# Performance work log

Measured on AMD Instinct MI355X. Metric: run time of the kernel, lower is better.

The kernel has to match this reference:

```python
import jax, jax.numpy as jnp
import numpy as np

IOU_TR = 0.3
SCORE_TR = 0.1
EPS = 1e-9
N_DET = 4096
N_CLASSES = 20


def setup_inputs() -> dict:
    key = jax.random.key(0)
    k1, k2, k3, k4 = jax.random.split(key, 4)
    scores = jax.random.uniform(k1, (N_DET,), dtype=jnp.float32)
    classes = jax.random.randint(k2, (N_DET,), 0, N_CLASSES).astype(jnp.float32)
    centers = jax.random.uniform(k3, (N_DET, 3), dtype=jnp.float32) * 64.0
    dims = jax.random.uniform(k4, (N_DET, 3), dtype=jnp.float32) * 8.0 + 1.0
    results = jnp.concatenate([scores[:, None], classes[:, None], centers, dims], axis=1)
    return {"results": results}


def _pairwise_iou3d(boxes):
    # boxes: [N, 6] = (cx, cy, cz, w, h, d) center format
    c = boxes[:, :3]
    d = boxes[:, 3:]
    lo = c - d * 0.5  # [N,3]
    hi = c + d * 0.5
    inter_lo = jnp.maximum(lo[:, None, :], lo[None, :, :])  # [N,N,3]
    inter_hi = jnp.minimum(hi[:, None, :], hi[None, :, :])
    inter = jnp.prod(jnp.clip(inter_hi - inter_lo, 0.0, None), axis=-1)  # [N,N]
    vol = jnp.prod(d, axis=-1)  # [N]
    union = vol[:, None] + vol[None, :] - inter
    return inter / (union + EPS)


def reference(results):
    # results: [N, 8] = (score, class, cx, cy, cz, w, h, d)
    N = results.shape[0]
    order = jnp.argsort(-results[:, 0])  # sort by score descending
    r = results[order]
    valid = r[:, 0] >= SCORE_TR  # score threshold filter
    iou = _pairwise_iou3d(r[:, 2:])  # [N,N]
    idx = jnp.arange(N)

    def body(i, state):
        keep, active = state
        cur = active[i]
        keep = keep.at[i].set(cur)
        # suppress later boxes whose IoU with box i exceeds threshold
        sup = cur & (iou[i] > IOU_TR) & (idx > i)
        active = active & (~sup)
        return keep, active

    keep, _ = jax.lax.fori_loop(0, N, body, (jnp.zeros(N, dtype=bool), valid))
    # static-shape output: suppressed / filtered rows zeroed instead of compacted
    return jnp.where(keep[:, None], r, jnp.zeros_like(r))
```

## Files before the change

### kernel.cpp

```cpp
#include <hip/hip_runtime.h>

typedef unsigned long long u64;
typedef unsigned int u32;
typedef unsigned short u16;

#define N_DET 4096
#define NW 64
#define IOU_TR 0.3f
#define SCORE_TR 0.1f
#define EPS 1e-9f


__device__ __forceinline__ u64 rl64(u64 v, int l) {
    unsigned lo = __builtin_amdgcn_readlane((unsigned)v, l);
    unsigned hi = __builtin_amdgcn_readlane((unsigned)(v >> 32), l);
    return ((u64)hi << 32) | lo;
}

__global__ void __launch_bounds__(256) k_sort(const float* __restrict__ res,
                                              float* __restrict__ rows,
                                              float* __restrict__ ssc,
                                              float4* __restrict__ soaLO,
                                              float4* __restrict__ soaHI,
                                              u64* __restrict__ A) {
    __shared__ float s[N_DET];
    int tid = threadIdx.x;
    if (blockIdx.x == 0 && tid < 64) A[tid] = 0ull;
    for (int j = tid; j < N_DET; j += 256) s[j] = res[j * 8];
    __syncthreads();
    int r = tid >> 4, c = tid & 15;
    int gi = blockIdx.x * 16 + r;
    float sc = s[gi];
    int part = 0;
    int j0 = c * 256;
    for (int j = j0; j < j0 + 256; ++j) {
        float sj = s[j];
        part += (sj > sc) || (sj == sc && j < gi);
    }
    part += __shfl_xor(part, 1, 64);
    part += __shfl_xor(part, 2, 64);
    part += __shfl_xor(part, 4, 64);
    part += __shfl_xor(part, 8, 64);
    if (c == 0) {
        int rank = part;
        float4 a = *(const float4*)(res + gi * 8);
        float4 b = *(const float4*)(res + gi * 8 + 4);
        *(float4*)(rows + rank * 8)     = a;
        *(float4*)(rows + rank * 8 + 4) = b;
        ssc[rank] = a.x;
        float cx = a.z, cy = a.w, cz = b.x, dx = b.y, dy = b.z, dz = b.w;
        soaLO[rank] = make_float4(cx - dx * 0.5f, cy - dy * 0.5f,
                                  cz - dz * 0.5f, (dx * dy) * dz);
        soaHI[rank] = make_float4(cx + dx * 0.5f, cy + dy * 0.5f,
                                  cz + dz * 0.5f, 0.0f);
    }
}

__global__ void k_sup(const float4* __restrict__ soaLO,
                      const float4* __restrict__ soaHI,
                      u64* __restrict__ Trm, u64* __restrict__ A) {
    int lane = threadIdx.x & 63;
    int wave = threadIdx.x >> 6;
    int i = blockIdx.x * 4 + wave;
    float4 iLO = soaLO[i];
    float4 iHI = soaHI[i];
    u64 rowword = 0, rowOr = 0;
    for (int w = (i >> 6); w < NW; ++w) {
        int j = w * 64 + lane;
        float4 jLO = soaLO[j];
        float4 jHI = soaHI[j];
        float ix = fminf(iHI.x, jHI.x) - fmaxf(iLO.x, jLO.x); ix = fmaxf(ix, 0.f);
        float iy = fminf(iHI.y, jHI.y) - fmaxf(iLO.y, jLO.y); iy = fmaxf(iy, 0.f);
        float iz = fminf(iHI.z, jHI.z) - fmaxf(iLO.z, jLO.z); iz = fmaxf(iz, 0.f);
        float inter = (ix * iy) * iz;
        float uni = iLO.w + jLO.w - inter;
        float iou = inter / (uni + EPS);
        bool sb = (iou > IOU_TR) && (j > i);
        u64 m = __ballot(sb);
        rowOr |= m;
        rowword = (lane == w) ? m : rowword;
    }
    if (rowOr) {
        Trm[(size_t)i * NW + lane] = rowword;
        if (lane == 0) atomicOr(&A[i >> 6], 1ull << (i & 63));
    }
}

#define FIDX(V, GB) { V = (u32)s_nlist[(GB) + (lane & 15)]; }

#define IS1(V, P, S) { u32 si_ = (u32)__builtin_amdgcn_readlane((V), (S)); \
    P##S = Trm[(size_t)si_ * NW + lane]; }

#define IS16(V, P) IS1(V,P,0) IS1(V,P,1) IS1(V,P,2) IS1(V,P,3)   \
    IS1(V,P,4) IS1(V,P,5) IS1(V,P,6) IS1(V,P,7)                  \
    IS1(V,P,8) IS1(V,P,9) IS1(V,P,10) IS1(V,P,11)                \
    IS1(V,P,12) IS1(V,P,13) IS1(V,P,14) IS1(V,P,15)

#define PR1(V, P, S) { u32 si_ = (u32)__builtin_amdgcn_readlane((V), (S)); \
    u64 awd_ = rl64(act, (int)(si_ >> 6));                                 \
    u64 bit_ = (awd_ >> (si_ & 63u)) & 1ull;                               \
    u64 m_ = (0ull - bit_) & (0ull - (u64)(si_ != 4095u));                 \
    act &= ~(P##S & m_); }

#define PR16(V, P) PR1(V,P,0) PR1(V,P,1) PR1(V,P,2) PR1(V,P,3)   \
    PR1(V,P,4) PR1(V,P,5) PR1(V,P,6) PR1(V,P,7)                  \
    PR1(V,P,8) PR1(V,P,9) PR1(V,P,10) PR1(V,P,11)                \
    PR1(V,P,12) PR1(V,P,13) PR1(V,P,14) PR1(V,P,15)

__global__ void __launch_bounds__(256, 1)
k_scan(const u64* __restrict__ Trm, const u64* __restrict__ A,
       const float* __restrict__ ssc, u64* __restrict__ keep) {
    __shared__ u64 s_valid[NW];
    __shared__ u16 s_nlist[4224];
    const int tid = threadIdx.x;
    const int wv = tid >> 6;
    const int lane = tid & 63;

    for (int w = wv * 16; w < wv * 16 + 16; ++w) {
        float scw = ssc[w * 64 + lane];
        u64 m = __ballot(scw >= SCORE_TR);
        if (lane == 0) s_valid[w] = m;
    }
    __syncthreads();
    if (wv != 0) return;

    u64 act = s_valid[lane];
    u64 avA = A[lane];
    int pc = __popcll(avA);
    int inc = pc;
#pragma unroll
    for (int d = 1; d < 64; d <<= 1) {
        int t = __shfl_up(inc, d, 64);
        if (lane >= d) inc += t;
    }
    int exc = inc - pc;
    int nTotal = __shfl(inc, 63, 64);
    {
        u64 m = avA; int o = exc;
        while (m) {
            int k = __builtin_ctzll(m); m &= m - 1;
            s_nlist[o++] = (u16)(lane * 64 + k);
        }
    }
    int padded = (nTotal + 63) & ~63;
    for (int t = nTotal + lane; t < padded + 128; t += 64)
        s_nlist[t] = (u16)4095;
    __threadfence_block();

    if (padded > 0) {
        u64 pa0,pa1,pa2,pa3,pa4,pa5,pa6,pa7,
            pa8,pa9,pa10,pa11,pa12,pa13,pa14,pa15;
        u64 pb0,pb1,pb2,pb3,pb4,pb5,pb6,pb7,
            pb8,pb9,pb10,pb11,pb12,pb13,pb14,pb15;
        u32 iA0, iA1, iB0, iB1;
        FIDX(iA0, 0)  IS16(iA0, pa)
        FIDX(iB0, 16) IS16(iB0, pb)
        int g = 0;
        while (g < padded) {
            FIDX(iA1, g + 32)
            PR16(iA0, pa)
            IS16(iA1, pa)
            FIDX(iB1, g + 48)
            PR16(iB0, pb)
            IS16(iB1, pb)
            g += 32;
            if (g >= padded) break;
            FIDX(iA0, g + 32)
            PR16(iA1, pa)
            IS16(iA0, pa)
            FIDX(iB0, g + 48)
            PR16(iB1, pb)
            IS16(iB0, pb)
            g += 32;
        }
    }
    keep[lane] = act;
}

__global__ void k_out(const float* __restrict__ rows,
                      const u64* __restrict__ keep,
                      float* __restrict__ out) {
    int i = blockIdx.x * 256 + threadIdx.x;
    bool kp = (keep[i >> 6] >> (i & 63)) & 1ull;
    float4 a = kp ? ((const float4*)rows)[i * 2]     : make_float4(0.f, 0.f, 0.f, 0.f);
    float4 b = kp ? ((const float4*)rows)[i * 2 + 1] : make_float4(0.f, 0.f, 0.f, 0.f);
    ((float4*)out)[i * 2]     = a;
    ((float4*)out)[i * 2 + 1] = b;
}

extern "C" void kernel_launch(void* const* d_in, const int* in_sizes, int n_in,
                              void* d_out, int out_size, void* d_ws, size_t ws_size,
                              hipStream_t stream) {
    const float* res = (const float*)d_in[0];
    float* out = (float*)d_out;

    float*  rows  = (float*)d_ws;
    float*  ssc   = rows + N_DET * 8;
    float4* soaLO = (float4*)(ssc + N_DET);
    float4* soaHI = soaLO + N_DET;
    u64*    A     = (u64*)(soaHI + N_DET);
    u64*    keep  = A + NW;
    u64*    Trm   = keep + NW;

    k_sort<<<N_DET / 16, 256, 0, stream>>>(res, rows, ssc, soaLO, soaHI, A);
    k_sup <<<N_DET / 4, 256, 0, stream>>>(soaLO, soaHI, Trm, A);
    k_scan<<<1, 256, 0, stream>>>(Trm, A, ssc, keep);
    k_out <<<16, 256, 0, stream>>>(rows, keep, out);
}
```

Baseline: 57.50 us.

## Skip low-score rows in suppression and batch scan updates with conflict check

k_sup now returns early for boxes below the score threshold, so about 10% fewer rows are processed and fewer rows are flagged in A. The scan drops inactive rows from the nonzero list and handles each group of 16 rows speculatively. It ORs together the masks of all currently active rows, checks whether any row in the group is itself suppressed by that combined mask, and only falls back to sequential processing when such an intra-group dependency exists. This shortens the serial readlane chain in the single-wave scan but adds a second pass of readlanes per batch. It also zeroes row 4095 of Trm so padding entries are harmless.

```diff
diff --git a/kernel.cpp b/kernel.cpp
--- a/kernel.cpp
+++ b/kernel.cpp
@@ -22,10 +22,15 @@
                                               float* __restrict__ ssc,
                                               float4* __restrict__ soaLO,
                                               float4* __restrict__ soaHI,
-                                              u64* __restrict__ A) {
+                                              u64* __restrict__ A,
+                                              u64* __restrict__ Trm) {
     __shared__ float s[N_DET];
     int tid = threadIdx.x;
-    if (blockIdx.x == 0 && tid < 64) A[tid] = 0ull;
+    if (blockIdx.x == 0) {
+        if (tid < 64) A[tid] = 0ull;
+        if (tid >= 64 && tid < 128)
+            Trm[(size_t)4095 * NW + (tid - 64)] = 0ull;
+    }
     for (int j = tid; j < N_DET; j += 256) s[j] = res[j * 8];
     __syncthreads();
     int r = tid >> 4, c = tid & 15;
@@ -58,10 +63,12 @@
 
 __global__ void k_sup(const float4* __restrict__ soaLO,
                       const float4* __restrict__ soaHI,
+                      const float* __restrict__ ssc,
                       u64* __restrict__ Trm, u64* __restrict__ A) {
     int lane = threadIdx.x & 63;
     int wave = threadIdx.x >> 6;
     int i = blockIdx.x * 4 + wave;
+    if (ssc[i] < SCORE_TR) return;
     float4 iLO = soaLO[i];
     float4 iHI = soaHI[i];
     u64 rowword = 0, rowOr = 0;
@@ -96,16 +103,37 @@
     IS1(V,P,8) IS1(V,P,9) IS1(V,P,10) IS1(V,P,11)                \
     IS1(V,P,12) IS1(V,P,13) IS1(V,P,14) IS1(V,P,15)
 
+#define TA1(V, P, S) { u32 si_ = (u32)__builtin_amdgcn_readlane((V), (S)); \
+    u64 aw_ = rl64(act, (int)(si_ >> 6));                                  \
+    u64 m_ = 0ull - ((aw_ >> (si_ & 63u)) & 1ull);                         \
+    applied |= ((P##S) & m_); }
+
+#define TC1(V, S) { u32 si_ = (u32)__builtin_amdgcn_readlane((V), (S)); \
+    u64 aw_ = rl64(applied, (int)(si_ >> 6));                           \
+    cfl |= (aw_ >> (si_ & 63u)) & 1ull; }
+
 #define PR1(V, P, S) { u32 si_ = (u32)__builtin_amdgcn_readlane((V), (S)); \
     u64 awd_ = rl64(act, (int)(si_ >> 6));                                 \
-    u64 bit_ = (awd_ >> (si_ & 63u)) & 1ull;                               \
-    u64 m_ = (0ull - bit_) & (0ull - (u64)(si_ != 4095u));                 \
+    u64 m_ = 0ull - ((awd_ >> (si_ & 63u)) & 1ull);                        \
     act &= ~(P##S & m_); }
 
-#define PR16(V, P) PR1(V,P,0) PR1(V,P,1) PR1(V,P,2) PR1(V,P,3)   \
-    PR1(V,P,4) PR1(V,P,5) PR1(V,P,6) PR1(V,P,7)                  \
-    PR1(V,P,8) PR1(V,P,9) PR1(V,P,10) PR1(V,P,11)                \
-    PR1(V,P,12) PR1(V,P,13) PR1(V,P,14) PR1(V,P,15)
+#define BATCH16(V, P) { \
+    u64 applied = 0ull, cfl = 0ull; \
+    TA1(V,P,0)  TA1(V,P,1)  TA1(V,P,2)  TA1(V,P,3)  \
+    TA1(V,P,4)  TA1(V,P,5)  TA1(V,P,6)  TA1(V,P,7)  \
+    TA1(V,P,8)  TA1(V,P,9)  TA1(V,P,10) TA1(V,P,11) \
+    TA1(V,P,12) TA1(V,P,13) TA1(V,P,14) TA1(V,P,15) \
+    TC1(V,0)  TC1(V,1)  TC1(V,2)  TC1(V,3)  \
+    TC1(V,4)  TC1(V,5)  TC1(V,6)  TC1(V,7)  \
+    TC1(V,8)  TC1(V,9)  TC1(V,10) TC1(V,11) \
+    TC1(V,12) TC1(V,13) TC1(V,14) TC1(V,15) \
+    if (cfl) {                       \
+        PR1(V,P,0)  PR1(V,P,1)  PR1(V,P,2)  PR1(V,P,3)  \
+        PR1(V,P,4)  PR1(V,P,5)  PR1(V,P,6)  PR1(V,P,7)  \
+        PR1(V,P,8)  PR1(V,P,9)  PR1(V,P,10) PR1(V,P,11) \
+        PR1(V,P,12) PR1(V,P,13) PR1(V,P,14) PR1(V,P,15) \
+    } else { \
+        act &= ~applied; } }
 
 __global__ void __launch_bounds__(256, 1)
 k_scan(const u64* __restrict__ Trm, const u64* __restrict__ A,
@@ -125,7 +153,7 @@
     if (wv != 0) return;
 
     u64 act = s_valid[lane];
-    u64 avA = A[lane];
+    u64 avA = A[lane] & act;
     int pc = __popcll(avA);
     int inc = pc;
 #pragma unroll
@@ -158,18 +186,18 @@
         int g = 0;
         while (g < padded) {
             FIDX(iA1, g + 32)
-            PR16(iA0, pa)
+            BATCH16(iA0, pa)
             IS16(iA1, pa)
             FIDX(iB1, g + 48)
-            PR16(iB0, pb)
+            BATCH16(iB0, pb)
             IS16(iB1, pb)
             g += 32;
             if (g >= padded) break;
             FIDX(iA0, g + 32)
-            PR16(iA1, pa)
+            BATCH16(iA1, pa)
             IS16(iA0, pa)
             FIDX(iB0, g + 48)
-            PR16(iB1, pb)
+            BATCH16(iB1, pb)
             IS16(iB0, pb)
             g += 32;
         }
@@ -202,8 +230,8 @@
     u64*    keep  = A + NW;
     u64*    Trm   = keep + NW;
 
-    k_sort<<<N_DET / 16, 256, 0, stream>>>(res, rows, ssc, soaLO, soaHI, A);
-    k_sup <<<N_DET / 4, 256, 0, stream>>>(soaLO, soaHI, Trm, A);
+    k_sort<<<N_DET / 16, 256, 0, stream>>>(res, rows, ssc, soaLO, soaHI, A, Trm);
+    k_sup <<<N_DET / 4, 256, 0, stream>>>(soaLO, soaHI, ssc, Trm, A);
     k_scan<<<1, 256, 0, stream>>>(Trm, A, ssc, keep);
     k_out <<<16, 256, 0, stream>>>(rows, keep, out);
 }
```

After: 58.02 us. About the same (+0.9%).

## Skip below-threshold boxes in suppression and deepen scan prefetch pipeline

Applied to the files above, without the earlier changes.

k_sup now returns early for rows whose score is below the threshold, so the row-building work and the Trm writes for those rows are skipped. k_scan also drops such rows from its candidate list. The sentinel index 4095 gets a zeroed Trm row, which removes the per-step sentinel mask from the serial loop. The scan's software pipeline goes from two to four register groups of 16 prefetched rows, so more loads are in flight ahead of the serial dependency chain, at the cost of higher register pressure.

```diff
diff --git a/kernel.cpp b/kernel.cpp
--- a/kernel.cpp
+++ b/kernel.cpp
@@ -22,10 +22,15 @@
                                               float* __restrict__ ssc,
                                               float4* __restrict__ soaLO,
                                               float4* __restrict__ soaHI,
-                                              u64* __restrict__ A) {
+                                              u64* __restrict__ A,
+                                              u64* __restrict__ Trm) {
     __shared__ float s[N_DET];
     int tid = threadIdx.x;
-    if (blockIdx.x == 0 && tid < 64) A[tid] = 0ull;
+    if (blockIdx.x == 0) {
+        if (tid < 64) A[tid] = 0ull;
+        if (tid >= 64 && tid < 128)
+            Trm[(size_t)4095 * NW + (tid - 64)] = 0ull;
+    }
     for (int j = tid; j < N_DET; j += 256) s[j] = res[j * 8];
     __syncthreads();
     int r = tid >> 4, c = tid & 15;
@@ -58,10 +63,12 @@
 
 __global__ void k_sup(const float4* __restrict__ soaLO,
                       const float4* __restrict__ soaHI,
+                      const float* __restrict__ ssc,
                       u64* __restrict__ Trm, u64* __restrict__ A) {
     int lane = threadIdx.x & 63;
     int wave = threadIdx.x >> 6;
     int i = blockIdx.x * 4 + wave;
+    if (ssc[i] < SCORE_TR) return;
     float4 iLO = soaLO[i];
     float4 iHI = soaHI[i];
     u64 rowword = 0, rowOr = 0;
@@ -98,8 +105,7 @@
 
 #define PR1(V, P, S) { u32 si_ = (u32)__builtin_amdgcn_readlane((V), (S)); \
     u64 awd_ = rl64(act, (int)(si_ >> 6));                                 \
-    u64 bit_ = (awd_ >> (si_ & 63u)) & 1ull;                               \
-    u64 m_ = (0ull - bit_) & (0ull - (u64)(si_ != 4095u));                 \
+    u64 m_ = 0ull - ((awd_ >> (si_ & 63u)) & 1ull);                        \
     act &= ~(P##S & m_); }
 
 #define PR16(V, P) PR1(V,P,0) PR1(V,P,1) PR1(V,P,2) PR1(V,P,3)   \
@@ -111,7 +117,7 @@
 k_scan(const u64* __restrict__ Trm, const u64* __restrict__ A,
        const float* __restrict__ ssc, u64* __restrict__ keep) {
     __shared__ u64 s_valid[NW];
-    __shared__ u16 s_nlist[4224];
+    __shared__ u16 s_nlist[4352];
     const int tid = threadIdx.x;
     const int wv = tid >> 6;
     const int lane = tid & 63;
@@ -125,7 +131,7 @@
     if (wv != 0) return;
 
     u64 act = s_valid[lane];
-    u64 avA = A[lane];
+    u64 avA = A[lane] & act;
     int pc = __popcll(avA);
     int inc = pc;
 #pragma unroll
@@ -143,7 +149,7 @@
         }
     }
     int padded = (nTotal + 63) & ~63;
-    for (int t = nTotal + lane; t < padded + 128; t += 64)
+    for (int t = nTotal + lane; t < padded + 192; t += 64)
         s_nlist[t] = (u16)4095;
     __threadfence_block();
 
@@ -152,26 +158,21 @@
             pa8,pa9,pa10,pa11,pa12,pa13,pa14,pa15;
         u64 pb0,pb1,pb2,pb3,pb4,pb5,pb6,pb7,
             pb8,pb9,pb10,pb11,pb12,pb13,pb14,pb15;
-        u32 iA0, iA1, iB0, iB1;
-        FIDX(iA0, 0)  IS16(iA0, pa)
-        FIDX(iB0, 16) IS16(iB0, pb)
+        u64 pc0,pc1,pc2,pc3,pc4,pc5,pc6,pc7,
+            pc8,pc9,pc10,pc11,pc12,pc13,pc14,pc15;
+        u64 pd0,pd1,pd2,pd3,pd4,pd5,pd6,pd7,
+            pd8,pd9,pd10,pd11,pd12,pd13,pd14,pd15;
+        u32 iA, iB, iC, iD;
+        FIDX(iA, 0)  IS16(iA, pa)
+        FIDX(iB, 16) IS16(iB, pb)
+        FIDX(iC, 32) IS16(iC, pc)
         int g = 0;
         while (g < padded) {
-            FIDX(iA1, g + 32)
-            PR16(iA0, pa)
-            IS16(iA1, pa)
-            FIDX(iB1, g + 48)
-            PR16(iB0, pb)
-            IS16(iB1, pb)
-            g += 32;
-            if (g >= padded) break;
-            FIDX(iA0, g + 32)
-            PR16(iA1, pa)
-            IS16(iA0, pa)
-            FIDX(iB0, g + 48)
-            PR16(iB1, pb)
-            IS16(iB0, pb)
-            g += 32;
+            FIDX(iD, g + 48)  PR16(iA, pa)  IS16(iD, pd)
+            FIDX(iA, g + 64)  PR16(iB, pb)  IS16(iA, pa)
+            FIDX(iB, g + 80)  PR16(iC, pc)  IS16(iB, pb)
+            FIDX(iC, g + 96)  PR16(iD, pd)  IS16(iC, pc)
+            g += 64;
         }
     }
     keep[lane] = act;
@@ -202,8 +203,8 @@
     u64*    keep  = A + NW;
     u64*    Trm   = keep + NW;
 
-    k_sort<<<N_DET / 16, 256, 0, stream>>>(res, rows, ssc, soaLO, soaHI, A);
-    k_sup <<<N_DET / 4, 256, 0, stream>>>(soaLO, soaHI, Trm, A);
+    k_sort<<<N_DET / 16, 256, 0, stream>>>(res, rows, ssc, soaLO, soaHI, A, Trm);
+    k_sup <<<N_DET / 4, 256, 0, stream>>>(soaLO, soaHI, ssc, Trm, A);
     k_scan<<<1, 256, 0, stream>>>(Trm, A, ssc, keep);
     k_out <<<16, 256, 0, stream>>>(rows, keep, out);
 }
```

Result: faster. 55.31 us (-3.8%).
